# Kernel tuning notes

Measured on AMD Instinct MI355X. Metric: run time of the kernel, lower is better.

Reference implementation:

```python
import jax, jax.numpy as jnp
import numpy as np


def _unfold(x, r):
    # x: [b, ch, h, w] -> [b, ch, k*k, h, w], zero-padded 3x3-style neighborhoods
    b, ch, h, w = x.shape
    k = 2 * r + 1
    xp = jnp.pad(x, ((0, 0), (0, 0), (r, r), (r, r)))
    patches = [xp[:, :, i:i + h, j:j + w] for i in range(k) for j in range(k)]
    return jnp.stack(patches, axis=2)


def setup_inputs() -> dict:
    key = jax.random.key(0)
    ks = jax.random.split(key, 6)
    b, c, h, w = 4, 128, 128, 128
    scale = 1.0 / np.sqrt(c)
    return {
        "feature0": jax.random.normal(ks[0], (b, c, h, w), jnp.float32),
        "flow": jax.random.normal(ks[1], (b, 2, h, w), jnp.float32),
        "q_w": jax.random.normal(ks[2], (c, c), jnp.float32) * scale,
        "q_b": jax.random.normal(ks[3], (c,), jnp.float32) * 0.01,
        "k_w": jax.random.normal(ks[4], (c, c), jnp.float32) * scale,
        "k_b": jax.random.normal(ks[5], (c,), jnp.float32) * 0.01,
        "local_window_attn": 1,
        "local_window_radius": 1,
    }


def reference(feature0, flow, q_w, q_b, k_w, k_b, local_window_attn, local_window_radius):
    b, c, h, w = feature0.shape
    inv_sqrt_c = 1.0 / jnp.sqrt(jnp.asarray(c, feature0.dtype))
    x = feature0.reshape(b, c, h * w).transpose(0, 2, 1)  # [b, hw, c]
    q = x @ q_w.T + q_b  # q_proj
    if local_window_attn:
        r = local_window_radius
        kf = x @ k_w.T + k_b  # k_proj applied to original feature
        kmap = kf.transpose(0, 2, 1).reshape(b, c, h, w)
        kwin = _unfold(kmap, r)      # [b, c, k2, h, w]
        fwin = _unfold(flow, r)      # [b, 2, k2, h, w]
        qmap = q.reshape(b, h, w, c)
        scores = jnp.einsum('bhwc,bckhw->bhwk', qmap, kwin) * inv_sqrt_c
        prob = jax.nn.softmax(scores, axis=-1)
        out = jnp.einsum('bhwk,bfkhw->bfhw', prob, fwin)  # [b, 2, h, w]
        return out
    else:
        # NOTE: faithful to source, key = k_proj(q_proj(x))
        key_ = q @ k_w.T + k_b
        value = flow.reshape(b, flow.shape[1], h * w).transpose(0, 2, 1)  # [b, hw, 2]
        scores = jnp.einsum('bnc,bmc->bnm', q, key_) * inv_sqrt_c
        prob = jax.nn.softmax(scores, axis=-1)
        out = jnp.einsum('bnm,bmf->bnf', prob, value)
        return out.reshape(b, h, w, value.shape[-1]).transpose(0, 3, 1, 2)
```

## Files before the change

### kernel.cpp

```cpp
#include <hip/hip_runtime.h>


#define HW 16384
#define NB 4
#define TOT (NB * HW)

typedef short bf16x8 __attribute__((ext_vector_type(8)));
typedef float f32x4 __attribute__((ext_vector_type(4)));

__device__ __forceinline__ unsigned short f2bf(float f) {
    unsigned u = __float_as_uint(f);
    return (unsigned short)((u + 0x7fffu + ((u >> 16) & 1u)) >> 16);
}
__device__ __forceinline__ float bf2f(unsigned short s) {
    return __uint_as_float(((unsigned)s) << 16);
}

__global__ void prep_kernel(const float* __restrict__ qw, const float* __restrict__ qb,
                            const float* __restrict__ kw, const float* __restrict__ kb,
                            unsigned short* __restrict__ Mh, unsigned short* __restrict__ Ml,
                            float* __restrict__ u, float* __restrict__ v,
                            float* __restrict__ dptr) {
    __shared__ float red[128];
    int bid = blockIdx.x, tid = threadIdx.x;
    if (bid < 16) {
        int ci = bid * 8 + (tid >> 5);
        int cj = (tid & 31) * 4;
        float4 acc = make_float4(0.f, 0.f, 0.f, 0.f);
#pragma unroll 4
        for (int co = 0; co < 128; ++co) {
            float qv = qw[co * 128 + ci];
            float4 kv = *(const float4*)(kw + co * 128 + cj);
            acc.x += qv * kv.x; acc.y += qv * kv.y;
            acc.z += qv * kv.z; acc.w += qv * kv.w;
        }
        int o = ci * 128 + cj;
        float a[4] = {acc.x, acc.y, acc.z, acc.w};
#pragma unroll
        for (int j = 0; j < 4; ++j) {
            unsigned short h = f2bf(a[j]);
            Mh[o + j] = h;
            Ml[o + j] = f2bf(a[j] - bf2f(h));
        }
    } else {
        int half = tid >> 7, t = tid & 127;
        const float* w  = half ? kw : qw;
        const float* bv = half ? qb : kb;
        float acc = 0.f;
#pragma unroll 4
        for (int co = 0; co < 128; ++co) acc += w[co * 128 + t] * bv[co];
        if (half) v[t] = acc; else u[t] = acc;
        if (!half) red[t] = qb[t] * kb[t];
        __syncthreads();
        if (tid == 0) {
            float dd = 0.f;
            for (int i = 0; i < 128; ++i) dd += red[i];
            *dptr = dd;
        }
    }
}

__global__ __launch_bounds__(256, 2)
void proj_kernel(const float* __restrict__ feat, const unsigned short* __restrict__ MhG,
                 const unsigned short* __restrict__ MlG,
                 const float* __restrict__ u, const float* __restrict__ v,
                 const float* __restrict__ dptr, float* __restrict__ y,
                 float* __restrict__ gam, float* __restrict__ del) {
    int tid = threadIdx.x;
    int lane = tid & 63;
    int cig = tid >> 6;
    int ci0 = cig * 32;
    int pxg = blockIdx.x;
    int P0 = pxg * 64;
    int b = P0 >> 14, p0 = P0 & (HW - 1);
    int m = lane & 15, q = lane >> 4;
    const float* xbase = feat + (size_t)b * 128 * HW + p0;

    f32x4 zero = {0.f, 0.f, 0.f, 0.f};
    f32x4 acc[2][4];
#pragma unroll
    for (int t = 0; t < 2; ++t)
#pragma unroll
        for (int s = 0; s < 4; ++s) acc[t][s] = zero;
    float gacc[4] = {0.f, 0.f, 0.f, 0.f};
    float dacc[4] = {0.f, 0.f, 0.f, 0.f};

#pragma unroll
    for (int kc = 0; kc < 4; ++kc) {
        int c0 = kc * 32;
        bf16x8 ah[2], al[2];
#pragma unroll
        for (int t = 0; t < 2; ++t) {
            int roff = (ci0 + t * 16 + m) * 128 + c0 + q * 8;
            ah[t] = *(const bf16x8*)(MhG + roff);
            al[t] = *(const bf16x8*)(MlG + roff);
        }
        float uj[8], vj[8];
        if (cig == 0) {
#pragma unroll
            for (int j = 0; j < 8; ++j) {
                uj[j] = u[c0 + q * 8 + j];
                vj[j] = v[c0 + q * 8 + j];
            }
        }
        bf16x8 bh[4], bl[4];
#pragma unroll
        for (int s = 0; s < 4; ++s) {
            const float* xp = xbase + (size_t)(c0 + q * 8) * HW + s * 16 + m;
            float xv[8];
#pragma unroll
            for (int j = 0; j < 8; ++j) xv[j] = xp[(size_t)j * HW];
            if (cig == 0) {
#pragma unroll
                for (int j = 0; j < 8; ++j) {
                    gacc[s] = fmaf(xv[j], uj[j], gacc[s]);
                    dacc[s] = fmaf(xv[j], vj[j], dacc[s]);
                }
            }
#pragma unroll
            for (int j = 0; j < 8; ++j) {
                unsigned short h = f2bf(xv[j]);
                bh[s][j] = (short)h;
                bl[s][j] = (short)f2bf(xv[j] - bf2f(h));
            }
        }
#pragma unroll
        for (int t = 0; t < 2; ++t)
#pragma unroll
            for (int s = 0; s < 4; ++s) {
                acc[t][s] = __builtin_amdgcn_mfma_f32_16x16x32_bf16(ah[t], bh[s], acc[t][s], 0, 0, 0);
                acc[t][s] = __builtin_amdgcn_mfma_f32_16x16x32_bf16(ah[t], bl[s], acc[t][s], 0, 0, 0);
                acc[t][s] = __builtin_amdgcn_mfma_f32_16x16x32_bf16(al[t], bh[s], acc[t][s], 0, 0, 0);
            }
    }

    if (cig == 0) {
        float dconst = *dptr;
#pragma unroll
        for (int s = 0; s < 4; ++s) {
            float g = gacc[s], dd = dacc[s];
            g += __shfl_xor(g, 16);  g += __shfl_xor(g, 32);
            dd += __shfl_xor(dd, 16); dd += __shfl_xor(dd, 32);
            if (q == 0) {
                gam[(size_t)b * HW + p0 + s * 16 + m] = g;
                del[(size_t)b * HW + p0 + s * 16 + m] = dd + dconst;
            }
        }
    }

    int rg = lane >> 4, col = lane & 15;
#pragma unroll
    for (int t = 0; t < 2; ++t)
#pragma unroll
        for (int s = 0; s < 4; ++s) {
            float* yp = y + ((size_t)b * 128 + ci0 + t * 16 + rg * 4) * HW + p0 + s * 16 + col;
#pragma unroll
            for (int r = 0; r < 4; ++r) yp[(size_t)r * HW] = acc[t][s][r];
        }
}

__global__ __launch_bounds__(256, 4)
void attn_partial_kernel(const float* __restrict__ feat, const float* __restrict__ y,
                         float* __restrict__ ps) {
    int tid = threadIdx.x;
    int blk = blockIdx.x;
    int cg = blk >> 6;
    int P = ((blk & 63) * 256 + tid) * 4;
    int b = P >> 14;
    int p = P & (HW - 1);
    const float* xb = feat + ((size_t)b * 128 + cg * 16) * HW + p;
    const float* yb = y + ((size_t)b * 128 + cg * 16) * HW + p;

    f32x4 s[9];
#pragma unroll
    for (int k = 0; k < 9; ++k) s[k] = (f32x4){0.f, 0.f, 0.f, 0.f};

#pragma unroll 2
    for (int c = 0; c < 16; ++c) {
        float4 xv = *(const float4*)(xb + (size_t)c * HW);
        const float* yc = yb + (size_t)c * HW;
#pragma unroll
        for (int dy = 0; dy < 3; ++dy) {
            const float* yr = yc + (dy - 1) * 128;
            float4 mm = *(const float4*)(yr);
            float lm = yr[-1];
            float rp = yr[4];
            int k = dy * 3;
            s[k][0] += xv.x * lm;    s[k][1] += xv.y * mm.x;
            s[k][2] += xv.z * mm.y;  s[k][3] += xv.w * mm.z;
            s[k+1][0] += xv.x * mm.x; s[k+1][1] += xv.y * mm.y;
            s[k+1][2] += xv.z * mm.z; s[k+1][3] += xv.w * mm.w;
            s[k+2][0] += xv.x * mm.y; s[k+2][1] += xv.y * mm.z;
            s[k+2][2] += xv.z * mm.w; s[k+2][3] += xv.w * rp;
        }
    }
    float* pso = ps + (size_t)cg * 9 * TOT + P;
#pragma unroll
    for (int k = 0; k < 9; ++k)
        *(f32x4*)(pso + (size_t)k * TOT) = s[k];
}

__global__ __launch_bounds__(256, 4)
void attn_final_kernel(const float* __restrict__ flow, const float* __restrict__ ps,
                       const float* __restrict__ gam, const float* __restrict__ del,
                       float* __restrict__ out) {
    int P = blockIdx.x * 256 + threadIdx.x;
    int b = P >> 14, p = P & (HW - 1);
    int row = p >> 7, col = p & 127;
    const float inv = 0.08838834764831845f;

    float g = gam[P];
    float sc[9];
    float mx = -1e30f;
#pragma unroll
    for (int k = 0; k < 9; ++k) {
        int dy = k / 3 - 1, dx = (k % 3) - 1;
        bool valid = ((unsigned)(row + dy) < 128u) && ((unsigned)(col + dx) < 128u);
        float ssum = 0.f;
#pragma unroll
        for (int cg = 0; cg < 8; ++cg) ssum += ps[(size_t)(cg * 9 + k) * TOT + P];
        int Pn = P + dy * 128 + dx;
        Pn = max(0, min(TOT - 1, Pn));
        float s = valid ? (ssum + g + del[Pn]) * inv : 0.f;
        sc[k] = s;
        mx = fmaxf(mx, s);
    }
    float e[9], sum = 0.f;
#pragma unroll
    for (int k = 0; k < 9; ++k) { e[k] = __expf(sc[k] - mx); sum += e[k]; }
    float rs = 1.f / sum;

    float o0 = 0.f, o1 = 0.f;
#pragma unroll
    for (int k = 0; k < 9; ++k) {
        int dy = k / 3 - 1, dx = (k % 3) - 1;
        bool valid = ((unsigned)(row + dy) < 128u) && ((unsigned)(col + dx) < 128u);
        float pr = valid ? e[k] * rs : 0.f;
        int fi0 = b * 2 * HW + p + dy * 128 + dx;
        fi0 = max(0, min(2 * TOT - 1, fi0));
        int fi1 = (b * 2 + 1) * HW + p + dy * 128 + dx;
        fi1 = max(0, min(2 * TOT - 1, fi1));
        o0 += pr * flow[fi0];
        o1 += pr * flow[fi1];
    }
    out[(size_t)(b * 2) * HW + p] = o0;
    out[(size_t)(b * 2 + 1) * HW + p] = o1;
}

extern "C" void kernel_launch(void* const* d_in, const int* in_sizes, int n_in,
                              void* d_out, int out_size, void* d_ws, size_t ws_size,
                              hipStream_t stream) {
    const float* feat = (const float*)d_in[0];
    const float* flow = (const float*)d_in[1];
    const float* qw = (const float*)d_in[2];
    const float* qb = (const float*)d_in[3];
    const float* kw = (const float*)d_in[4];
    const float* kb = (const float*)d_in[5];

    float* ws = (float*)d_ws;
    float* u = ws;
    float* v = ws + 128;
    float* dptr = ws + 256;
    unsigned short* Mh = (unsigned short*)(ws + 512);
    unsigned short* Ml = (unsigned short*)(ws + 8704);
    float* y = ws + 16896;
    float* ps = ws + 8405760;
    float* gam = ws + 13124352;
    float* del = ws + 13189888;
    float* out = (float*)d_out;

    prep_kernel<<<17, 256, 0, stream>>>(qw, qb, kw, kb, Mh, Ml, u, v, dptr);
    proj_kernel<<<1024, 256, 0, stream>>>(feat, Mh, Ml, u, v, dptr, y, gam, del);
    attn_partial_kernel<<<512, 256, 0, stream>>>(feat, y, ps);
    attn_final_kernel<<<256, 256, 0, stream>>>(flow, ps, gam, del, out);
}
```

Before: 133.4 us.

## Fuse partial attention scores and softmax into one kernel with LDS reduction

Merges the partial-score kernel and the final softmax kernel into one. Each block of 512 threads splits the channel groups across 8 waves for 256 positions and reduces the partials through shared memory, so the large partial-score buffer is never written to or read back from global memory. The cost is fewer blocks (256 blocks of 512 threads with launch bounds of one block) and half the threads idle during the softmax phase, which lowers parallelism and latency hiding.

After: 134.8 us. No clear change (+1.0%).

```diff
diff --git a/kernel.cpp b/kernel.cpp
--- a/kernel.cpp
+++ b/kernel.cpp
@@ -159,17 +159,20 @@
         }
 }
 
-__global__ __launch_bounds__(256, 4)
-void attn_partial_kernel(const float* __restrict__ feat, const float* __restrict__ y,
-                         float* __restrict__ ps) {
+__global__ __launch_bounds__(512, 1)
+void attn_fused_kernel(const float* __restrict__ feat, const float* __restrict__ y,
+                       const float* __restrict__ gam, const float* __restrict__ del,
+                       const float* __restrict__ flow, float* __restrict__ out) {
+    __shared__ float sred[4][9][256];
+
     int tid = threadIdx.x;
-    int blk = blockIdx.x;
-    int cg = blk >> 6;
-    int P = ((blk & 63) * 256 + tid) * 4;
-    int b = P >> 14;
-    int p = P & (HW - 1);
-    const float* xb = feat + ((size_t)b * 128 + cg * 16) * HW + p;
-    const float* yb = y + ((size_t)b * 128 + cg * 16) * HW + p;
+    int wid = tid >> 6, lane = tid & 63;
+    int P0 = blockIdx.x * 256;
+    int P = P0 + lane * 4;
+    int b = P >> 14, p = P & (HW - 1);
+    int c0 = wid * 16;
+    const float* xb = feat + ((size_t)b * 128 + c0) * HW + p;
+    const float* yb = y + ((size_t)b * 128 + c0) * HW + p;
 
     f32x4 s[9];
 #pragma unroll
@@ -186,65 +189,73 @@
             float lm = yr[-1];
             float rp = yr[4];
             int k = dy * 3;
-            s[k][0] += xv.x * lm;    s[k][1] += xv.y * mm.x;
-            s[k][2] += xv.z * mm.y;  s[k][3] += xv.w * mm.z;
+            s[k][0] += xv.x * lm;     s[k][1] += xv.y * mm.x;
+            s[k][2] += xv.z * mm.y;   s[k][3] += xv.w * mm.z;
             s[k+1][0] += xv.x * mm.x; s[k+1][1] += xv.y * mm.y;
             s[k+1][2] += xv.z * mm.z; s[k+1][3] += xv.w * mm.w;
             s[k+2][0] += xv.x * mm.y; s[k+2][1] += xv.y * mm.z;
             s[k+2][2] += xv.z * mm.w; s[k+2][3] += xv.w * rp;
         }
     }
-    float* pso = ps + (size_t)cg * 9 * TOT + P;
-#pragma unroll
-    for (int k = 0; k < 9; ++k)
-        *(f32x4*)(pso + (size_t)k * TOT) = s[k];
-}
-
-__global__ __launch_bounds__(256, 4)
-void attn_final_kernel(const float* __restrict__ flow, const float* __restrict__ ps,
-                       const float* __restrict__ gam, const float* __restrict__ del,
-                       float* __restrict__ out) {
-    int P = blockIdx.x * 256 + threadIdx.x;
-    int b = P >> 14, p = P & (HW - 1);
-    int row = p >> 7, col = p & 127;
-    const float inv = 0.08838834764831845f;
-
-    float g = gam[P];
-    float sc[9];
-    float mx = -1e30f;
-#pragma unroll
-    for (int k = 0; k < 9; ++k) {
-        int dy = k / 3 - 1, dx = (k % 3) - 1;
-        bool valid = ((unsigned)(row + dy) < 128u) && ((unsigned)(col + dx) < 128u);
-        float ssum = 0.f;
-#pragma unroll
-        for (int cg = 0; cg < 8; ++cg) ssum += ps[(size_t)(cg * 9 + k) * TOT + P];
-        int Pn = P + dy * 128 + dx;
-        Pn = max(0, min(TOT - 1, Pn));
-        float s = valid ? (ssum + g + del[Pn]) * inv : 0.f;
-        sc[k] = s;
-        mx = fmaxf(mx, s);
-    }
-    float e[9], sum = 0.f;
-#pragma unroll
-    for (int k = 0; k < 9; ++k) { e[k] = __expf(sc[k] - mx); sum += e[k]; }
-    float rs = 1.f / sum;
-
-    float o0 = 0.f, o1 = 0.f;
-#pragma unroll
-    for (int k = 0; k < 9; ++k) {
-        int dy = k / 3 - 1, dx = (k % 3) - 1;
-        bool valid = ((unsigned)(row + dy) < 128u) && ((unsigned)(col + dx) < 128u);
-        float pr = valid ? e[k] * rs : 0.f;
-        int fi0 = b * 2 * HW + p + dy * 128 + dx;
-        fi0 = max(0, min(2 * TOT - 1, fi0));
-        int fi1 = (b * 2 + 1) * HW + p + dy * 128 + dx;
-        fi1 = max(0, min(2 * TOT - 1, fi1));
-        o0 += pr * flow[fi0];
-        o1 += pr * flow[fi1];
-    }
-    out[(size_t)(b * 2) * HW + p] = o0;
-    out[(size_t)(b * 2 + 1) * HW + p] = o1;
+
+    if (wid >= 4) {
+#pragma unroll
+        for (int k = 0; k < 9; ++k)
+            *(f32x4*)&sred[wid - 4][k][lane * 4] = s[k];
+    }
+    __syncthreads();
+    if (wid < 4) {
+#pragma unroll
+        for (int k = 0; k < 9; ++k) {
+            f32x4 t = *(const f32x4*)&sred[wid][k][lane * 4];
+            t += s[k];
+            *(f32x4*)&sred[wid][k][lane * 4] = t;
+        }
+    }
+    __syncthreads();
+
+    if (tid < 256) {
+        int Pf = P0 + tid;
+        int bf_ = Pf >> 14, pf = Pf & (HW - 1);
+        int row = pf >> 7, col = pf & 127;
+        const float inv = 0.08838834764831845f;
+        float g = gam[Pf];
+
+        float sc[9];
+        float mx = -1e30f;
+#pragma unroll
+        for (int k = 0; k < 9; ++k) {
+            int dy = k / 3 - 1, dx = (k % 3) - 1;
+            bool valid = ((unsigned)(row + dy) < 128u) && ((unsigned)(col + dx) < 128u);
+            float ssum = sred[0][k][tid] + sred[1][k][tid]
+                       + sred[2][k][tid] + sred[3][k][tid];
+            int Pn = Pf + dy * 128 + dx;
+            Pn = max(0, min(TOT - 1, Pn));
+            float sv = valid ? (ssum + g + del[Pn]) * inv : 0.f;
+            sc[k] = sv;
+            mx = fmaxf(mx, sv);
+        }
+        float e[9], sum = 0.f;
+#pragma unroll
+        for (int k = 0; k < 9; ++k) { e[k] = __expf(sc[k] - mx); sum += e[k]; }
+        float rs = 1.f / sum;
+
+        float o0 = 0.f, o1 = 0.f;
+#pragma unroll
+        for (int k = 0; k < 9; ++k) {
+            int dy = k / 3 - 1, dx = (k % 3) - 1;
+            bool valid = ((unsigned)(row + dy) < 128u) && ((unsigned)(col + dx) < 128u);
+            float pr = valid ? e[k] * rs : 0.f;
+            int fi0 = bf_ * 2 * HW + pf + dy * 128 + dx;
+            fi0 = max(0, min(2 * TOT - 1, fi0));
+            int fi1 = (bf_ * 2 + 1) * HW + pf + dy * 128 + dx;
+            fi1 = max(0, min(2 * TOT - 1, fi1));
+            o0 += pr * flow[fi0];
+            o1 += pr * flow[fi1];
+        }
+        out[(size_t)(bf_ * 2) * HW + pf] = o0;
+        out[(size_t)(bf_ * 2 + 1) * HW + pf] = o1;
+    }
 }
 
 extern "C" void kernel_launch(void* const* d_in, const int* in_sizes, int n_in,
@@ -264,13 +275,11 @@
     unsigned short* Mh = (unsigned short*)(ws + 512);
     unsigned short* Ml = (unsigned short*)(ws + 8704);
     float* y = ws + 16896;
-    float* ps = ws + 8405760;
-    float* gam = ws + 13124352;
-    float* del = ws + 13189888;
+    float* gam = ws + 8405760;
+    float* del = ws + 8471296;
     float* out = (float*)d_out;
 
     prep_kernel<<<17, 256, 0, stream>>>(qw, qb, kw, kb, Mh, Ml, u, v, dptr);
     proj_kernel<<<1024, 256, 0, stream>>>(feat, Mh, Ml, u, v, dptr, y, gam, del);
-    attn_partial_kernel<<<512, 256, 0, stream>>>(feat, y, ps);
-    attn_final_kernel<<<256, 256, 0, stream>>>(flow, ps, gam, del, out);
-}
+    attn_fused_kernel<<<256, 512, 0, stream>>>(feat, y, gam, del, flow, out);
+}
```
